# Optimization experiments

Measured on AMD Instinct MI355X. Metric: run time of the kernel, lower is better.

The kernel has to match this reference:

```python
import jax, jax.numpy as jnp
import numpy as np

NUM_HEADS = 8      # SD1.x UNet cross-attn heads at 64x64 block
NUM_PROMPTS = 4    # batch = 2*NUM_PROMPTS (uncond + cond CFG halves)


def setup_inputs() -> dict:
    key = jax.random.key(0)
    ks = jax.random.split(key, 8)
    B, T, C = 2 * NUM_PROMPTS, 4096, 320   # spatial tokens, inner dim
    S, D = 77, 768                          # CLIP text seq len / width
    return {
        "hidden_states": jax.random.normal(ks[0], (B, T, C), jnp.float32),
        "encoder_hidden_states": jax.random.normal(ks[1], (B, S, D), jnp.float32),
        "mapper": jax.random.uniform(ks[2], (NUM_PROMPTS - 1, S, S), jnp.float32),
        "Wq": jax.random.normal(ks[3], (C, C), jnp.float32) * 0.02,
        "Wk": jax.random.normal(ks[4], (D, C), jnp.float32) * 0.02,
        "Wv": jax.random.normal(ks[5], (D, C), jnp.float32) * 0.02,
        "Wo": jax.random.normal(ks[6], (C, C), jnp.float32) * 0.02,
        "bo": jnp.zeros((C,), jnp.float32),
    }


def reference(hidden_states, encoder_hidden_states, mapper, Wq, Wk, Wv, Wo, bo):
    B, T, C = hidden_states.shape
    S = encoder_hidden_states.shape[1]
    H = NUM_HEADS
    d = C // H
    scale = 1.0 / jnp.sqrt(jnp.asarray(d, hidden_states.dtype))

    # projections + head split (diffusers head_to_batch_dim layout)
    q = (hidden_states @ Wq).reshape(B, T, H, d)
    k = (encoder_hidden_states @ Wk).reshape(B, S, H, d)
    v = (encoder_hidden_states @ Wv).reshape(B, S, H, d)

    # full attention probabilities must be materialized for the P2P swap
    scores = jnp.einsum('bthd,bshd->bhts', q, k) * scale
    probs = jax.nn.softmax(scores, axis=-1)  # [B, H, T, S]

    # conditional (CFG) half: [P, H, T, S]; swap via mapper einsum (cross-attn,
    # cur_step < num_steps_cross branch of swap_attention_probs)
    half = B // 2
    uncond = probs[:half]
    cond = probs[half:]
    attn_base = cond[0]                                   # [H, T, S]
    replaced = jnp.einsum('htm,pme->phte', attn_base, mapper)  # [P-1, H, T, S]
    cond = jnp.concatenate([attn_base[None], replaced], axis=0)
    probs = jnp.concatenate([uncond, cond], axis=0)

    # value matmul + merge heads (batch_to_head_dim) + output projection
    out = jnp.einsum('bhts,bshd->bthd', probs, v).reshape(B, T, C)
    return out @ Wo + bo
```

## Files before the change

kernel.cpp:

```cpp
#include <hip/hip_runtime.h>
#include <hip/hip_bf16.h>

typedef unsigned short ushort;
typedef __attribute__((ext_vector_type(8))) short bf16x8;
typedef __attribute__((ext_vector_type(8))) unsigned short ushort8;
typedef __attribute__((ext_vector_type(4))) float f32x4;
typedef __attribute__((ext_vector_type(4))) float float4v;

__device__ __forceinline__ ushort f2bf(float f) {
    union { float f; unsigned u; } v; v.f = f;
    unsigned r = v.u + 0x7FFFu + ((v.u >> 16) & 1u);
    return (ushort)(r >> 16);
}
__device__ __forceinline__ float bf2f(ushort u) {
    union { unsigned u; float f; } v; v.u = ((unsigned)u) << 16;
    return v.f;
}

#define KF_SZ   (5u * 8 * 5 * 2 * 512)
#define VF_SZ   (5u * 8 * 3 * 3 * 512)
#define VPF_SZ  (3u * 8 * 3 * 3 * 512)
#define WF_SZ   (10u * 2 * 10 * 512)

__global__ __launch_bounds__(256) void prep_k(
    const float* __restrict__ Wq, const float* __restrict__ Wk,
    const float* __restrict__ Wv, const float* __restrict__ Wo,
    ushort* __restrict__ Wq_t, ushort* __restrict__ Wk_t,
    ushort* __restrict__ Wv_t, ushort* __restrict__ Wo_t,
    ushort* __restrict__ Kf, ushort* __restrict__ Vf, ushort* __restrict__ VPf)
{
    int b = blockIdx.x;
    if (b >= 680) {
        const ushort8 z8 = {0,0,0,0,0,0,0,0};
        unsigned i = (b - 680) * 256 + threadIdx.x;
        if (i < KF_SZ / 8) ((ushort8*)Kf)[i] = z8;
        else if (i < (KF_SZ + VF_SZ) / 8) ((ushort8*)Vf)[i - KF_SZ / 8] = z8;
        else if (i < (KF_SZ + VF_SZ + VPF_SZ) / 8) ((ushort8*)VPf)[i - (KF_SZ + VF_SZ) / 8] = z8;
        return;
    }
    __shared__ ushort t[32][33];
    const float* src; ushort* dst; int K; int tb;
    if (b < 100)      { src = Wq; dst = Wq_t; K = 320; tb = b; }
    else if (b < 340) { src = Wk; dst = Wk_t; K = 768; tb = b - 100; }
    else if (b < 580) { src = Wv; dst = Wv_t; K = 768; tb = b - 340; }
    else              { src = Wo; dst = Wo_t; K = 320; tb = b - 580; }
    int tc = tb % 10, tr = tb / 10;
    int tx = threadIdx.x & 31, ty = threadIdx.x >> 5;
    #pragma unroll
    for (int p = 0; p < 4; ++p) {
        int k = tr * 32 + ty + p * 8, n = tc * 32 + tx;
        t[ty + p * 8][tx] = f2bf(src[(size_t)k * 320 + n]);
    }
    __syncthreads();
    #pragma unroll
    for (int p = 0; p < 4; ++p) {
        int n = tc * 32 + ty + p * 8, k = tr * 32 + tx;
        dst[(size_t)n * K + k] = t[tx][ty + p * 8];
    }
}

__global__ __launch_bounds__(256) void gemm_kv(
    const float* __restrict__ E, const ushort* __restrict__ Wk_t,
    const ushort* __restrict__ Wv_t, const ushort* __restrict__ Wq_t,
    const ushort* __restrict__ Wo_t,
    float* __restrict__ part, ushort* __restrict__ Wof, ushort* __restrict__ Wqf)
{
    const int tid = threadIdx.x;
    const int bid = blockIdx.x;
    if (bid >= 160) {
        int i = (bid - 160) * 256 + tid;
        const ushort* src; ushort* dst;
        if (i < 12800) { src = Wo_t; dst = Wof; }
        else           { src = Wq_t; dst = Wqf; i -= 12800; }
        int g = i >> 6, l = i & 63;
        int kk = g / 20, half = (g / 10) & 1, f = g % 10;
        int n = half * 160 + f * 16 + (l & 15);
        int k0 = kk * 32 + (l >> 4) * 8;
        *(ushort8*)(dst + (size_t)g * 512 + l * 8) =
            *(const ushort8*)(src + (size_t)n * 320 + k0);
        return;
    }
    __shared__ ushort A_lds[2][64 * 40];
    __shared__ ushort B_lds[2][320 * 40];
    const int w = tid >> 6, l = tid & 63;
    const int c15 = l & 15, khi = (l >> 4) * 8;
    const int r = tid >> 2, p = (tid & 3) * 8;
    const int rbase = (l >> 4) * 4;
    f32x4 acc[4][5] = {};

    const int mtile = bid % 10, mat = (bid / 10) & 1, ks = bid / 20;
    const int m0 = mtile * 64, kk0 = ks * 96;
    const ushort* Bt = mat ? Wv_t : Wk_t;
    const int m = m0 + r;
    const bool live = (m < 616);
    const float* Abase = E + (size_t)(live ? m : 0) * 768 + p;
    float4v a0 = {0,0,0,0}, a1 = {0,0,0,0};
    ushort8 breg[5];
    if (live) { a0 = *(const float4v*)(Abase + kk0); a1 = *(const float4v*)(Abase + kk0 + 4); }
    #pragma unroll
    for (int i = 0; i < 5; ++i) {
        int idx = tid + i * 256; int n = idx >> 2, q = (idx & 3) * 8;
        breg[i] = *(const ushort8*)(Bt + (size_t)n * 768 + kk0 + q);
    }
    {
        ushort* d = &A_lds[0][r * 40 + p];
        d[0]=f2bf(a0.x); d[1]=f2bf(a0.y); d[2]=f2bf(a0.z); d[3]=f2bf(a0.w);
        d[4]=f2bf(a1.x); d[5]=f2bf(a1.y); d[6]=f2bf(a1.z); d[7]=f2bf(a1.w);
        #pragma unroll
        for (int i = 0; i < 5; ++i) {
            int idx = tid + i * 256; int n = idx >> 2, q = (idx & 3) * 8;
            *(ushort8*)&B_lds[0][n * 40 + q] = breg[i];
        }
    }
    __syncthreads();
    for (int k = 0; k < 3; ++k) {
        const int cur = k & 1;
        if (k < 2) {
            int kk = kk0 + (k + 1) * 32;
            if (live) { a0 = *(const float4v*)(Abase + kk); a1 = *(const float4v*)(Abase + kk + 4); }
            #pragma unroll
            for (int i = 0; i < 5; ++i) {
                int idx = tid + i * 256; int n = idx >> 2, q = (idx & 3) * 8;
                breg[i] = *(const ushort8*)(Bt + (size_t)n * 768 + kk + q);
            }
        }
        bf16x8 a[4];
        #pragma unroll
        for (int mf = 0; mf < 4; ++mf)
            a[mf] = *(const bf16x8*)&A_lds[cur][(mf * 16 + c15) * 40 + khi];
        #pragma unroll
        for (int f = 0; f < 5; ++f) {
            bf16x8 b = *(const bf16x8*)&B_lds[cur][(w * 80 + f * 16 + c15) * 40 + khi];
            #pragma unroll
            for (int mf = 0; mf < 4; ++mf)
                acc[mf][f] = __builtin_amdgcn_mfma_f32_16x16x32_bf16(a[mf], b, acc[mf][f], 0, 0, 0);
        }
        if (k < 2) {
            const int nxt = cur ^ 1;
            ushort* d = &A_lds[nxt][r * 40 + p];
            d[0]=f2bf(a0.x); d[1]=f2bf(a0.y); d[2]=f2bf(a0.z); d[3]=f2bf(a0.w);
            d[4]=f2bf(a1.x); d[5]=f2bf(a1.y); d[6]=f2bf(a1.z); d[7]=f2bf(a1.w);
            #pragma unroll
            for (int i = 0; i < 5; ++i) {
                int idx = tid + i * 256; int n = idx >> 2, q = (idx & 3) * 8;
                *(ushort8*)&B_lds[nxt][n * 40 + q] = breg[i];
            }
            __syncthreads();
        }
    }
    float* dst = part + (size_t)(mat * 8 + ks) * 640 * 320;
    #pragma unroll
    for (int mf = 0; mf < 4; ++mf)
        #pragma unroll
        for (int f = 0; f < 5; ++f) {
            int col = w * 80 + f * 16 + c15;
            #pragma unroll
            for (int rr = 0; rr < 4; ++rr)
                dst[(size_t)(m0 + mf * 16 + rbase + rr) * 320 + col] = acc[mf][f][rr];
        }
}

__global__ __launch_bounds__(256) void kv_reduce(
    const float* __restrict__ part, ushort* __restrict__ Kf,
    ushort* __restrict__ Vf, ushort* __restrict__ VVt)
{
    int idx = blockIdx.x * 256 + threadIdx.x;
    if (idx >= 616 * 320) return;
    int mat = blockIdx.y;
    int row = idx / 320, col = idx - row * 320;
    float s8 = 0.f;
    #pragma unroll
    for (int ks = 0; ks < 8; ++ks)
        s8 += part[((size_t)(mat * 8 + ks) * 640 + row) * 320 + col];
    ushort b = f2bf(s8);
    int bt = row / 77, s = row - bt * 77;
    int h = col / 40, kd = col - h * 40;
    if (mat == 0) {
        if (bt < 5) {
            int kt = kd >> 5, chunk = (kd >> 3) & 3;
            int lane = (s & 15) | (chunk << 4);
            Kf[((size_t)((bt * 8 + h) * 5 + (s >> 4)) * 2 + kt) * 512 + lane * 8 + (kd & 7)] = b;
        }
    } else {
        if (bt < 5) {
            int lane = (kd & 15) | (((s >> 3) & 3) << 4);
            Vf[(((size_t)(bt * 8 + h) * 3 + (kd >> 4)) * 3 + (s >> 5)) * 512 + lane * 8 + (s & 7)] = b;
        } else {
            VVt[((size_t)bt * 320 + col) * 80 + s] = b;
        }
    }
}

__global__ void vprime_k(const float* __restrict__ mapper, const ushort* __restrict__ VVt,
                         ushort* __restrict__ VPf)
{
    int pm = blockIdx.x;
    int p = pm / 77, m = pm - p * 77;
    __shared__ float mp[77];
    int tid = threadIdx.x;
    if (tid < 77) mp[tid] = mapper[(size_t)pm * 77 + tid];
    __syncthreads();
    const ushort* vrow = VVt + ((size_t)(5 + p) * 320 + tid) * 80;
    float acc = 0.f;
    for (int e = 0; e < 77; ++e) acc += mp[e] * bf2f(vrow[e]);
    int h = tid / 40, dc = tid - h * 40;
    int lane = (dc & 15) | (((m >> 3) & 3) << 4);
    VPf[(((size_t)(p * 8 + h) * 3 + (dc >> 4)) * 3 + (m >> 5)) * 512 + lane * 8 + (m & 7)] = f2bf(acc);
}

#define ATT_SCALE 0.15811388300841897f
__global__ __launch_bounds__(512, 4) void attn_out_k(
    const float* __restrict__ hs, const ushort* __restrict__ Wqf,
    const ushort* __restrict__ Kf, const ushort* __restrict__ Vf,
    const ushort* __restrict__ VPf, const ushort* __restrict__ Wof,
    const float* __restrict__ bias, float* __restrict__ out)
{
    __shared__ __align__(16) ushort AO_lds[64 * 328];
    __shared__ __align__(16) ushort P_lds[8 * 16 * 104];

    const int tid = threadIdx.x;
    const int ww = tid >> 6, l = tid & 63;
    const int rg = ww & 3, half = ww >> 2;
    const int c15 = l & 15, hi4 = l >> 4;
    const int khi = hi4 * 8, rbase = hi4 * 4;
    const int bt = blockIdx.y, t0 = blockIdx.x * 64;
    const int qb = (bt < 5) ? bt : 4;
    const ushort* Vfb = (bt < 5) ? (Vf + (size_t)bt * (8 * 3 * 3 * 512))
                                 : (VPf + (size_t)(bt - 5) * (8 * 3 * 3 * 512));
    const ushort8 z8 = {0,0,0,0,0,0,0,0};
    ushort* Pw = P_lds + ww * (16 * 104);

    if (l < 48) {
        int r = l / 3, c = l - 3 * (l / 3);
        *(ushort8*)&Pw[r * 104 + 80 + c * 8] = z8;
    }

    for (int i = tid; i < 2560; i += 512) {
        int r = i / 40, cc = i - (i / 40) * 40;
        const float4v* s = (const float4v*)(hs + (size_t)(qb * 4096 + t0 + r) * 320 + cc * 8);
        float4v x0 = s[0], x1 = s[1];
        ushort* d = &AO_lds[r * 328 + cc * 8];
        d[0]=f2bf(x0.x); d[1]=f2bf(x0.y); d[2]=f2bf(x0.z); d[3]=f2bf(x0.w);
        d[4]=f2bf(x1.x); d[5]=f2bf(x1.y); d[6]=f2bf(x1.z); d[7]=f2bf(x1.w);
    }
    __syncthreads();

    const int cb = half * 160;
    {
        f32x4 qacc[10] = {};
        for (int kk = 0; kk < 10; ++kk) {
            bf16x8 a = *(const bf16x8*)&AO_lds[(rg * 16 + c15) * 328 + kk * 32 + khi];
            const ushort* wb = Wqf + (size_t)((kk * 2 + half) * 10) * 512 + l * 8;
            #pragma unroll
            for (int f = 0; f < 10; ++f)
                qacc[f] = __builtin_amdgcn_mfma_f32_16x16x32_bf16(
                    a, *(const bf16x8*)(wb + (size_t)f * 512), qacc[f], 0, 0, 0);
        }
        __syncthreads();
        #pragma unroll
        for (int f = 0; f < 10; ++f) {
            int col = cb + f * 16 + c15;
            #pragma unroll
            for (int rr = 0; rr < 4; ++rr)
                AO_lds[(rg * 16 + rbase + rr) * 328 + col] = f2bf(qacc[f][rr]);
        }
    }

    for (int hh = 0; hh < 4; ++hh) {
        const int h = half * 4 + hh;

        bf16x8 qa0 = *(const bf16x8*)&AO_lds[(rg * 16 + c15) * 328 + h * 40 + khi];
        bf16x8 qa1 = {0,0,0,0,0,0,0,0};
        if (hi4 == 0) qa1 = *(const bf16x8*)&AO_lds[(rg * 16 + c15) * 328 + h * 40 + 32];

        f32x4 sacc[5] = {};
        #pragma unroll
        for (int f = 0; f < 5; ++f) {
            const ushort* kfb = Kf + ((size_t)((qb * 8 + h) * 5 + f) * 2) * 512 + l * 8;
            bf16x8 kb0 = *(const bf16x8*)(kfb);
            bf16x8 kb1 = *(const bf16x8*)(kfb + 512);
            sacc[f] = __builtin_amdgcn_mfma_f32_16x16x32_bf16(qa0, kb0, sacc[f], 0, 0, 0);
            sacc[f] = __builtin_amdgcn_mfma_f32_16x16x32_bf16(qa1, kb1, sacc[f], 0, 0, 0);
        }

        bf16x8 vreg[3][3];
        #pragma unroll
        for (int f = 0; f < 3; ++f)
            #pragma unroll
            for (int kt = 0; kt < 3; ++kt)
                vreg[f][kt] = *(const bf16x8*)(Vfb + (((size_t)(h * 3 + f) * 3 + kt)) * 512 + l * 8);

        float pv[5][4];
        #pragma unroll
        for (int r = 0; r < 4; ++r) {
            float sum = 0.f;
            #pragma unroll
            for (int f = 0; f < 5; ++f) {
                bool valid = (f < 4) || (c15 < 13);
                float e = valid ? __expf(sacc[f][r] * ATT_SCALE) : 0.f;
                pv[f][r] = e; sum += e;
            }
            #pragma unroll
            for (int d = 1; d < 16; d <<= 1) sum += __shfl_xor(sum, d);
            float inv = 1.f / sum;
            #pragma unroll
            for (int f = 0; f < 5; ++f) pv[f][r] *= inv;
        }

        #pragma unroll
        for (int r = 0; r < 4; ++r)
            #pragma unroll
            for (int f = 0; f < 5; ++f)
                Pw[(rbase + r) * 104 + f * 16 + c15] = f2bf(pv[f][r]);

        bf16x8 pa[3];
        #pragma unroll
        for (int kt = 0; kt < 3; ++kt)
            pa[kt] = *(const bf16x8*)&Pw[c15 * 104 + kt * 32 + khi];
        f32x4 oacc[3] = {};
        #pragma unroll
        for (int f = 0; f < 3; ++f)
            #pragma unroll
            for (int kt = 0; kt < 3; ++kt)
                oacc[f] = __builtin_amdgcn_mfma_f32_16x16x32_bf16(pa[kt], vreg[f][kt], oacc[f], 0, 0, 0);

        #pragma unroll
        for (int f = 0; f < 3; ++f) {
            int col = f * 16 + c15;
            if (col < 40) {
                #pragma unroll
                for (int r = 0; r < 4; ++r)
                    AO_lds[(rg * 16 + rbase + r) * 328 + h * 40 + col] = f2bf(oacc[f][r]);
            }
        }
    }
    __syncthreads();

    f32x4 acc[10] = {};
    for (int kk = 0; kk < 10; ++kk) {
        bf16x8 a = *(const bf16x8*)&AO_lds[(rg * 16 + c15) * 328 + kk * 32 + khi];
        const ushort* wb = Wof + (size_t)((kk * 2 + half) * 10) * 512 + l * 8;
        #pragma unroll
        for (int f = 0; f < 10; ++f) {
            bf16x8 b = *(const bf16x8*)(wb + (size_t)f * 512);
            acc[f] = __builtin_amdgcn_mfma_f32_16x16x32_bf16(a, b, acc[f], 0, 0, 0);
        }
    }

    #pragma unroll
    for (int f = 0; f < 10; ++f) {
        int col = cb + f * 16 + c15;
        #pragma unroll
        for (int rr = 0; rr < 4; ++rr)
            out[(size_t)(bt * 4096 + t0 + rg * 16 + rbase + rr) * 320 + col]
                = acc[f][rr] + bias[col];
    }
}

extern "C" void kernel_launch(void* const* d_in, const int* in_sizes, int n_in,
                              void* d_out, int out_size, void* d_ws, size_t ws_size,
                              hipStream_t stream) {
    (void)in_sizes; (void)n_in; (void)out_size; (void)ws_size;
    const float* hs     = (const float*)d_in[0];
    const float* ehs    = (const float*)d_in[1];
    const float* mapper = (const float*)d_in[2];
    const float* Wq     = (const float*)d_in[3];
    const float* Wk     = (const float*)d_in[4];
    const float* Wv     = (const float*)d_in[5];
    const float* Wo     = (const float*)d_in[6];
    const float* bo     = (const float*)d_in[7];
    float* out = (float*)d_out;

    ushort* ws   = (ushort*)d_ws;
    ushort* Wq_t = ws;
    ushort* Wk_t = Wq_t + 320 * 320;
    ushort* Wv_t = Wk_t + 320 * 768;
    ushort* Wo_t = Wv_t + 320 * 768;
    ushort* Wof  = Wo_t + 320 * 320;
    ushort* Wqf  = Wof + WF_SZ;
    ushort* Kfb  = Wqf + WF_SZ;
    ushort* Vfb  = Kfb + KF_SZ;
    ushort* VPfb = Vfb + VF_SZ;
    ushort* VVt  = VPfb + VPF_SZ;
    float*  part = (float*)(VVt + 8 * 320 * 80);

    prep_k<<<1069, 256, 0, stream>>>(Wq, Wk, Wv, Wo, Wq_t, Wk_t, Wv_t, Wo_t,
                                     Kfb, Vfb, VPfb);
    gemm_kv<<<260, 256, 0, stream>>>(ehs, Wk_t, Wv_t, Wq_t, Wo_t, part, Wof, Wqf);
    kv_reduce<<<dim3(770, 2), 256, 0, stream>>>(part, Kfb, Vfb, VVt);
    vprime_k<<<231, 320, 0, stream>>>(mapper, VVt, VPfb);
    attn_out_k<<<dim3(64, 8), 512, 0, stream>>>(hs, Wqf, Kfb, Vfb, VPfb, Wof, bo, out);
}
```

Before: 74.44 us.

## Stage Wq/Wo tiles through LDS and assign one head per wave

The Q and output projections now cooperatively copy each 32-row weight slab into shared memory (reusing the P buffer) and read MFMA B-operands from LDS instead of each wave loading from global. The attention phase is remapped so each wave owns one head across all four row groups, which lets K fragments be loaded once into registers and reused. V fragments are loaded per row group inside the loop. This is meant to cut redundant global and L2 traffic, at the cost of extra block-wide barriers per k-step and more register pressure from holding K.

```diff
diff --git a/kernel.cpp b/kernel.cpp
--- a/kernel.cpp
+++ b/kernel.cpp
@@ -217,10 +217,10 @@
 {
     __shared__ __align__(16) ushort AO_lds[64 * 328];
     __shared__ __align__(16) ushort P_lds[8 * 16 * 104];
+    ushort* W_lds = P_lds;
 
     const int tid = threadIdx.x;
     const int ww = tid >> 6, l = tid & 63;
-    const int rg = ww & 3, half = ww >> 2;
     const int c15 = l & 15, hi4 = l >> 4;
     const int khi = hi4 * 8, rbase = hi4 * 4;
     const int bt = blockIdx.y, t0 = blockIdx.x * 64;
@@ -229,11 +229,8 @@
                                  : (VPf + (size_t)(bt - 5) * (8 * 3 * 3 * 512));
     const ushort8 z8 = {0,0,0,0,0,0,0,0};
     ushort* Pw = P_lds + ww * (16 * 104);
-
-    if (l < 48) {
-        int r = l / 3, c = l - 3 * (l / 3);
-        *(ushort8*)&Pw[r * 104 + 80 + c * 8] = z8;
-    }
+    const int rg = ww & 3, half = ww >> 2;
+    const int cb = half * 160;
 
     for (int i = tid; i < 2560; i += 512) {
         int r = i / 40, cc = i - (i / 40) * 40;
@@ -245,18 +242,23 @@
     }
     __syncthreads();
 
-    const int cb = half * 160;
     {
         f32x4 qacc[10] = {};
         for (int kk = 0; kk < 10; ++kk) {
+            const ushort* wsrc = Wqf + (size_t)kk * 10240;
+            int c0 = tid, c1 = tid + 512, c2 = tid + 1024;
+            *(ushort8*)&W_lds[c0 * 8] = *(const ushort8*)(wsrc + c0 * 8);
+            *(ushort8*)&W_lds[c1 * 8] = *(const ushort8*)(wsrc + c1 * 8);
+            if (c2 < 1280) *(ushort8*)&W_lds[c2 * 8] = *(const ushort8*)(wsrc + c2 * 8);
+            __syncthreads();
             bf16x8 a = *(const bf16x8*)&AO_lds[(rg * 16 + c15) * 328 + kk * 32 + khi];
-            const ushort* wb = Wqf + (size_t)((kk * 2 + half) * 10) * 512 + l * 8;
-            #pragma unroll
-            for (int f = 0; f < 10; ++f)
-                qacc[f] = __builtin_amdgcn_mfma_f32_16x16x32_bf16(
-                    a, *(const bf16x8*)(wb + (size_t)f * 512), qacc[f], 0, 0, 0);
-        }
-        __syncthreads();
+            #pragma unroll
+            for (int f = 0; f < 10; ++f) {
+                bf16x8 b = *(const bf16x8*)&W_lds[(half * 10 + f) * 512 + l * 8];
+                qacc[f] = __builtin_amdgcn_mfma_f32_16x16x32_bf16(a, b, qacc[f], 0, 0, 0);
+            }
+            __syncthreads();
+        }
         #pragma unroll
         for (int f = 0; f < 10; ++f) {
             int col = cb + f * 16 + c15;
@@ -265,30 +267,32 @@
                 AO_lds[(rg * 16 + rbase + rr) * 328 + col] = f2bf(qacc[f][rr]);
         }
     }
-
-    for (int hh = 0; hh < 4; ++hh) {
-        const int h = half * 4 + hh;
-
-        bf16x8 qa0 = *(const bf16x8*)&AO_lds[(rg * 16 + c15) * 328 + h * 40 + khi];
+    __syncthreads();
+
+    const int h = ww;
+    if (l < 48) {
+        int r = l / 3, c = l - 3 * (l / 3);
+        *(ushort8*)&Pw[r * 104 + 80 + c * 8] = z8;
+    }
+    bf16x8 kreg[5][2];
+    #pragma unroll
+    for (int f = 0; f < 5; ++f) {
+        const ushort* kfb = Kf + ((size_t)((qb * 8 + h) * 5 + f) * 2) * 512 + l * 8;
+        kreg[f][0] = *(const bf16x8*)(kfb);
+        kreg[f][1] = *(const bf16x8*)(kfb + 512);
+    }
+
+    for (int rg4 = 0; rg4 < 4; ++rg4) {
+        bf16x8 qa0 = *(const bf16x8*)&AO_lds[(rg4 * 16 + c15) * 328 + h * 40 + khi];
         bf16x8 qa1 = {0,0,0,0,0,0,0,0};
-        if (hi4 == 0) qa1 = *(const bf16x8*)&AO_lds[(rg * 16 + c15) * 328 + h * 40 + 32];
+        if (hi4 == 0) qa1 = *(const bf16x8*)&AO_lds[(rg4 * 16 + c15) * 328 + h * 40 + 32];
 
         f32x4 sacc[5] = {};
         #pragma unroll
         for (int f = 0; f < 5; ++f) {
-            const ushort* kfb = Kf + ((size_t)((qb * 8 + h) * 5 + f) * 2) * 512 + l * 8;
-            bf16x8 kb0 = *(const bf16x8*)(kfb);
-            bf16x8 kb1 = *(const bf16x8*)(kfb + 512);
-            sacc[f] = __builtin_amdgcn_mfma_f32_16x16x32_bf16(qa0, kb0, sacc[f], 0, 0, 0);
-            sacc[f] = __builtin_amdgcn_mfma_f32_16x16x32_bf16(qa1, kb1, sacc[f], 0, 0, 0);
-        }
-
-        bf16x8 vreg[3][3];
-        #pragma unroll
-        for (int f = 0; f < 3; ++f)
-            #pragma unroll
-            for (int kt = 0; kt < 3; ++kt)
-                vreg[f][kt] = *(const bf16x8*)(Vfb + (((size_t)(h * 3 + f) * 3 + kt)) * 512 + l * 8);
+            sacc[f] = __builtin_amdgcn_mfma_f32_16x16x32_bf16(qa0, kreg[f][0], sacc[f], 0, 0, 0);
+            sacc[f] = __builtin_amdgcn_mfma_f32_16x16x32_bf16(qa1, kreg[f][1], sacc[f], 0, 0, 0);
+        }
 
         float pv[5][4];
         #pragma unroll
@@ -317,12 +321,18 @@
         #pragma unroll
         for (int kt = 0; kt < 3; ++kt)
             pa[kt] = *(const bf16x8*)&Pw[c15 * 104 + kt * 32 + khi];
-        f32x4 oacc[3] = {};
-        #pragma unroll
-        for (int f = 0; f < 3; ++f)
-            #pragma unroll
-            for (int kt = 0; kt < 3; ++kt)
-                oacc[f] = __builtin_amdgcn_mfma_f32_16x16x32_bf16(pa[kt], vreg[f][kt], oacc[f], 0, 0, 0);
+        f32x4 oacc[3];
+        #pragma unroll
+        for (int f = 0; f < 3; ++f) {
+            bf16x8 v0 = *(const bf16x8*)(Vfb + (((size_t)(h * 3 + f) * 3 + 0)) * 512 + l * 8);
+            bf16x8 v1 = *(const bf16x8*)(Vfb + (((size_t)(h * 3 + f) * 3 + 1)) * 512 + l * 8);
+            bf16x8 v2 = *(const bf16x8*)(Vfb + (((size_t)(h * 3 + f) * 3 + 2)) * 512 + l * 8);
+            f32x4 o = {};
+            o = __builtin_amdgcn_mfma_f32_16x16x32_bf16(pa[0], v0, o, 0, 0, 0);
+            o = __builtin_amdgcn_mfma_f32_16x16x32_bf16(pa[1], v1, o, 0, 0, 0);
+            o = __builtin_amdgcn_mfma_f32_16x16x32_bf16(pa[2], v2, o, 0, 0, 0);
+            oacc[f] = o;
+        }
 
         #pragma unroll
         for (int f = 0; f < 3; ++f) {
@@ -330,7 +340,7 @@
             if (col < 40) {
                 #pragma unroll
                 for (int r = 0; r < 4; ++r)
-                    AO_lds[(rg * 16 + rbase + r) * 328 + h * 40 + col] = f2bf(oacc[f][r]);
+                    AO_lds[(rg4 * 16 + rbase + r) * 328 + h * 40 + col] = f2bf(oacc[f][r]);
             }
         }
     }
@@ -338,13 +348,21 @@
 
     f32x4 acc[10] = {};
     for (int kk = 0; kk < 10; ++kk) {
+        const ushort* wsrc = Wof + (size_t)kk * 10240;
+        {
+            int c0 = tid, c1 = tid + 512, c2 = tid + 1024;
+            *(ushort8*)&W_lds[c0 * 8] = *(const ushort8*)(wsrc + c0 * 8);
+            *(ushort8*)&W_lds[c1 * 8] = *(const ushort8*)(wsrc + c1 * 8);
+            if (c2 < 1280) *(ushort8*)&W_lds[c2 * 8] = *(const ushort8*)(wsrc + c2 * 8);
+        }
+        __syncthreads();
         bf16x8 a = *(const bf16x8*)&AO_lds[(rg * 16 + c15) * 328 + kk * 32 + khi];
-        const ushort* wb = Wof + (size_t)((kk * 2 + half) * 10) * 512 + l * 8;
         #pragma unroll
         for (int f = 0; f < 10; ++f) {
-            bf16x8 b = *(const bf16x8*)(wb + (size_t)f * 512);
+            bf16x8 b = *(const bf16x8*)&W_lds[(half * 10 + f) * 512 + l * 8];
             acc[f] = __builtin_amdgcn_mfma_f32_16x16x32_bf16(a, b, acc[f], 0, 0, 0);
         }
+        if (kk < 9) __syncthreads();
     }
 
     #pragma unroll
```

New measurement: 65.65 us. -11.8%, faster.
